# Kernel optimization log

Measured on AMD Instinct MI355X. Metric: run time of the kernel, lower is better.

The kernel has to match this reference:

```python
import jax, jax.numpy as jnp
import numpy as np

BETA = 0.25
N_E = 256
E_DIM = 1024


def setup_inputs() -> dict:
    key = jax.random.key(0)
    k1, k2, k3, k4 = jax.random.split(key, 4)
    z = jax.random.normal(k1, (16, E_DIM, 32, 32), dtype=jnp.float32)
    emb = jax.random.normal(k2, (N_E, E_DIM), dtype=jnp.float32)
    conv_w = jax.random.normal(k3, (E_DIM, E_DIM), dtype=jnp.float32) * 0.02
    conv_b = jax.random.normal(k4, (E_DIM,), dtype=jnp.float32) * 0.02
    return {"z": z, "emb": emb, "conv_w": conv_w, "conv_b": conv_b}


def reference(z, emb, conv_w, conv_b):
    # z: [B, C=e_dim, H, W] -> channels-last, flatten spatial+batch
    zp = jnp.transpose(z, (0, 2, 3, 1))          # [B, H, W, C]
    zf = zp.reshape(-1, E_DIM)                    # [N, C]
    # squared L2 distances to codebook: [N, n_e]
    d = (jnp.sum(zf * zf, axis=1, keepdims=True)
         + jnp.sum(emb * emb, axis=1)
         - 2.0 * (zf @ emb.T))
    min_idx = jnp.argmin(d, axis=1)               # [N]
    min_enc = jax.nn.one_hot(min_idx, N_E, dtype=z.dtype)  # [N, n_e]
    z_q = (min_enc @ emb).reshape(zp.shape)       # gather via matmul, as original
    # VQ commitment loss with straight-through estimator
    loss = (jnp.mean((jax.lax.stop_gradient(z_q) - zp) ** 2)
            + BETA * jnp.mean((z_q - jax.lax.stop_gradient(zp)) ** 2))
    z_q = zp + jax.lax.stop_gradient(z_q - zp)
    e_mean = jnp.mean(min_enc, axis=0)
    perplexity = jnp.exp(-jnp.sum(e_mean * jnp.log(e_mean + 1e-10)))
    # back to channels-first, then 1x1 conv (= per-pixel GEMM)
    z_q = jnp.transpose(z_q, (0, 3, 1, 2))        # [B, C, H, W]
    out = jnp.einsum('bchw,oc->bohw', z_q, conv_w) + conv_b[None, :, None, None]
    return out, loss, perplexity, min_idx
```

## Files before the change

kernel.cpp:

```cpp
#include <hip/hip_runtime.h>
#include <math.h>

#define NE 256
#define EDIM 1024
#define HW 1024
#define NPIX 16384
#define OUT_ELEMS 16777216

typedef short short8 __attribute__((ext_vector_type(8)));
typedef float f32x4 __attribute__((ext_vector_type(4)));

#define WS_HIST   0
#define WS_LOSS   1024
#define WS_ZSQ    1028
#define WS_FBITS  2048
#define WS_T      4096
#define WS_MEMSET 1052672
#define WS_CE2    1052672
#define WS_IDX    1053696
#define WS_EH     1119232
#define WS_EL     1643520
#define WS_NEED   2167808

#define DELTA 0.02f

#define WO_CE2  0
#define WO_HIST 1024
#define WO_LOSS 2048
#define WO_IDX  4096
#define WO_T    69632
#define WO_TOTAL 1118208

__device__ __forceinline__ unsigned short f2bf(float f) {
    unsigned u = __float_as_uint(f);
    unsigned r = u + 0x7FFFu + ((u >> 16) & 1u);
    return (unsigned short)(r >> 16);
}
__device__ __forceinline__ float bf2f(unsigned short h) {
    return __uint_as_float(((unsigned)h) << 16);
}

__device__ __forceinline__ void stage16(const void* g, void* l) {
    __builtin_amdgcn_global_load_lds(
        (const __attribute__((address_space(1))) unsigned int*)g,
        (__attribute__((address_space(3))) unsigned int*)l, 16, 0, 0);
}

__global__ __launch_bounds__(64) void k_prep(const float* __restrict__ emb,
                                             unsigned short* __restrict__ eh,
                                             unsigned short* __restrict__ el,
                                             float* __restrict__ ce2) {
    int j = blockIdx.x;
    int l = threadIdx.x;
    const float* row = emb + ((size_t)j << 10);
    float s = 0.f;
    #pragma unroll
    for (int i = 0; i < 4; i++) {
        float4 v = *(const float4*)(row + l * 4 + 256 * i);
        s += v.x * v.x + v.y * v.y + v.z * v.z + v.w * v.w;
        unsigned short h0 = f2bf(v.x), h1 = f2bf(v.y), h2 = f2bf(v.z), h3 = f2bf(v.w);
        uint2 hp, lp;
        hp.x = (unsigned)h0 | ((unsigned)h1 << 16);
        hp.y = (unsigned)h2 | ((unsigned)h3 << 16);
        lp.x = (unsigned)f2bf(v.x - bf2f(h0)) | ((unsigned)f2bf(v.y - bf2f(h1)) << 16);
        lp.y = (unsigned)f2bf(v.z - bf2f(h2)) | ((unsigned)f2bf(v.w - bf2f(h3)) << 16);
        *(uint2*)(eh + ((size_t)j << 10) + l * 4 + 256 * i) = hp;
        *(uint2*)(el + ((size_t)j << 10) + l * 4 + 256 * i) = lp;
    }
    #pragma unroll
    for (int m = 32; m; m >>= 1) s += __shfl_down(s, m, 64);
    if (l == 0) ce2[j] = 0.5f * s;
}

__global__ __launch_bounds__(256) void k_wT(const float* __restrict__ w,
                                            const float* __restrict__ emb,
                                            float* __restrict__ T) {
    __shared__ float wt[64 * 17];
    __shared__ float et[64 * 17];
    int t = threadIdx.x;
    int j0 = blockIdx.x * 64;
    int o0 = blockIdx.y * 64;
    int kb = blockIdx.z * 256;
    int to = t & 15, tj = t >> 4;
    float acc[4][4] = {};
    int lr = t >> 2, lk = (t & 3) * 4;
    for (int kk = kb; kk < kb + 256; kk += 16) {
        float4 wv = *(const float4*)(w + (size_t)(o0 + lr) * EDIM + kk + lk);
        float4 ev = *(const float4*)(emb + (size_t)(j0 + lr) * EDIM + kk + lk);
        __syncthreads();
        wt[lr * 17 + lk + 0] = wv.x; wt[lr * 17 + lk + 1] = wv.y;
        wt[lr * 17 + lk + 2] = wv.z; wt[lr * 17 + lk + 3] = wv.w;
        et[lr * 17 + lk + 0] = ev.x; et[lr * 17 + lk + 1] = ev.y;
        et[lr * 17 + lk + 2] = ev.z; et[lr * 17 + lk + 3] = ev.w;
        __syncthreads();
        #pragma unroll
        for (int k = 0; k < 16; k++) {
            float a[4], b[4];
            #pragma unroll
            for (int i = 0; i < 4; i++) a[i] = wt[(to * 4 + i) * 17 + k];
            #pragma unroll
            for (int i = 0; i < 4; i++) b[i] = et[(tj * 4 + i) * 17 + k];
            #pragma unroll
            for (int i = 0; i < 4; i++)
                #pragma unroll
                for (int jx = 0; jx < 4; jx++) acc[i][jx] += a[i] * b[jx];
        }
    }
    #pragma unroll
    for (int i = 0; i < 4; i++)
        #pragma unroll
        for (int jx = 0; jx < 4; jx++)
            atomicAdd(&T[(size_t)(o0 + to * 4 + i) * NE + j0 + tj * 4 + jx],
                      acc[i][jx]);
}

__global__ __launch_bounds__(256) void k_dist(
        const float* __restrict__ z, const unsigned short* __restrict__ eh,
        const unsigned short* __restrict__ el,
        const float* __restrict__ ce2,
        int* __restrict__ idx_i, float* __restrict__ idx_f,
        int* __restrict__ hist, float* __restrict__ loss_s,
        float* __restrict__ zsq_acc, unsigned int* __restrict__ fbits) {
    __shared__ unsigned short sB[4][2][256 * 32];
    int t = threadIdx.x;
    int lane = t & 63, w = t >> 6;
    int m = lane & 15, quad = lane >> 4;
    int px0 = blockIdx.x * 64;
    int b = px0 >> 10;
    const float* zp = z + (((size_t)b) << 20) + (px0 & 1023) + w * 16 + m;
    int sc = t >> 2, qp = t & 3;
    int ql = qp ^ ((sc >> 1) & 3);

    f32x4 acc[16];
    #pragma unroll
    for (int nt = 0; nt < 16; nt++) acc[nt] = (f32x4){0.f, 0.f, 0.f, 0.f};

    float zv0[8], zv1[8], zv2[8], zv3[8];
    float zsq = 0.f;
    int sq = quad ^ ((m >> 1) & 3);

#define STAGE(c, B) do {                                                        \
    int kk_ = (c) * 32;                                                         \
    _Pragma("unroll")                                                           \
    for (int i_ = 0; i_ < 4; i_++) {                                            \
        stage16(eh + (((size_t)(i_ * 64 + sc)) << 10) + kk_ + ql * 8,           \
                &sB[B][0][(i_ * 256 + w * 64) * 8]);                            \
        stage16(el + (((size_t)(i_ * 64 + sc)) << 10) + kk_ + ql * 8,           \
                &sB[B][1][(i_ * 256 + w * 64) * 8]);                            \
    } } while (0)

#define ZLOAD(c, ZV) do {                                                       \
    int kk_ = (c) * 32;                                                         \
    _Pragma("unroll")                                                           \
    for (int j_ = 0; j_ < 8; j_++)                                              \
        ZV[j_] = zp[((size_t)(kk_ + quad * 8 + j_)) << 10];                     \
    } while (0)

#define WAITV(n) do {                                                           \
    asm volatile("s_waitcnt vmcnt(" #n ")" ::: "memory");                       \
    __builtin_amdgcn_sched_barrier(0); } while (0)

#define FENCE() do {                                                            \
    asm volatile("" ::: "memory");                                              \
    __builtin_amdgcn_sched_barrier(0); } while (0)

#define BODY(c, B, ZV, PRE, B3, ZV3) do {                                       \
    __builtin_amdgcn_s_barrier();                                               \
    short8 ah, al;                                                              \
    _Pragma("unroll")                                                           \
    for (int j_ = 0; j_ < 8; j_++) {                                            \
        float zj_ = ZV[j_];                                                     \
        zsq += zj_ * zj_;                                                       \
        unsigned short h_ = f2bf(zj_);                                          \
        ((unsigned short*)&ah)[j_] = h_;                                        \
        ((unsigned short*)&al)[j_] = f2bf(zj_ - bf2f(h_));                      \
    }                                                                           \
    if (PRE) { STAGE((c) + 3, B3); ZLOAD((c) + 3, ZV3); }                       \
    _Pragma("unroll")                                                           \
    for (int nt_ = 0; nt_ < 16; nt_++) {                                        \
        short8 bh_ = *(const short8*)&sB[B][0][(nt_ * 16 + m) * 32 + sq * 8];   \
        short8 bl_ = *(const short8*)&sB[B][1][(nt_ * 16 + m) * 32 + sq * 8];   \
        acc[nt_] = __builtin_amdgcn_mfma_f32_16x16x32_bf16(ah, bh_, acc[nt_], 0, 0, 0); \
        acc[nt_] = __builtin_amdgcn_mfma_f32_16x16x32_bf16(ah, bl_, acc[nt_], 0, 0, 0); \
        acc[nt_] = __builtin_amdgcn_mfma_f32_16x16x32_bf16(al, bh_, acc[nt_], 0, 0, 0); \
    } } while (0)

    STAGE(0, 0); ZLOAD(0, zv0); FENCE();
    STAGE(1, 1); ZLOAD(1, zv1); FENCE();
    STAGE(2, 2); ZLOAD(2, zv2);

    for (int mi = 0; mi < 7; mi++) {
        WAITV(32); BODY(mi * 4 + 0, 0, zv0, 1, 3, zv3);
        WAITV(32); BODY(mi * 4 + 1, 1, zv1, 1, 0, zv0);
        WAITV(32); BODY(mi * 4 + 2, 2, zv2, 1, 1, zv1);
        WAITV(32); BODY(mi * 4 + 3, 3, zv3, 1, 2, zv2);
    }
    WAITV(32); BODY(28, 0, zv0, 1, 3, zv3);
    WAITV(32); BODY(29, 1, zv1, 0, 2, zv2);
    WAITV(16); BODY(30, 2, zv2, 0, 3, zv3);
    WAITV(0);  BODY(31, 3, zv3, 0, 0, zv0);

#undef STAGE
#undef ZLOAD
#undef WAITV
#undef FENCE
#undef BODY

    #pragma unroll
    for (int msk = 32; msk; msk >>= 1) zsq += __shfl_down(zsq, msk, 64);
    if (lane == 0) atomicAdd(zsq_acc, zsq);

    float c2v[16];
    #pragma unroll
    for (int nt = 0; nt < 16; nt++) c2v[nt] = ce2[nt * 16 + m];

    float lsum = 0.f;
    #pragma unroll
    for (int r = 0; r < 4; r++) {
        float v1 = 3.4e38f, v2 = 3.4e38f; int i1 = 0;
        #pragma unroll
        for (int nt = 0; nt < 16; nt++) {
            int code = nt * 16 + m;
            float sv = c2v[nt] - acc[nt][r];
            if (sv < v1 || (sv == v1 && code < i1)) { v2 = v1; v1 = sv; i1 = code; }
            else v2 = fminf(v2, sv);
        }
        #pragma unroll
        for (int msk = 1; msk < 16; msk <<= 1) {
            float ov1 = __shfl_xor(v1, msk, 64);
            int   oi1 = __shfl_xor(i1, msk, 64);
            float ov2 = __shfl_xor(v2, msk, 64);
            float nv2 = fminf(fminf(v2, ov2), fmaxf(v1, ov1));
            if (ov1 < v1 || (ov1 == v1 && oi1 < i1)) { v1 = ov1; i1 = oi1; }
            v2 = nv2;
        }
        if (m == 0) {
            int px = px0 + w * 16 + quad * 4 + r;
            idx_i[px] = i1;
            idx_f[px] = (float)i1;
            atomicAdd(&hist[i1], 1);
            if (v2 - v1 < DELTA)
                atomicOr(&fbits[px >> 5], 1u << (px & 31));
            lsum += v1;
        }
    }
    lsum += __shfl_xor(lsum, 16, 64);
    lsum += __shfl_xor(lsum, 32, 64);
    if (lane == 0) atomicAdd(loss_s, lsum);
}

__global__ __launch_bounds__(256) void k_cleanup(const float* __restrict__ z,
        const float* __restrict__ emb, const float* __restrict__ ce2,
        const unsigned int* __restrict__ fbits,
        int* __restrict__ idx_i, float* __restrict__ idx_f, int* __restrict__ hist) {
    __shared__ float zs[1024];
    __shared__ float rv[4];
    __shared__ int ri[4];
    int t = threadIdx.x;
    const float* er = emb + (size_t)t * EDIM;
    for (int px = blockIdx.x; px < NPIX; px += gridDim.x) {
        if (!(fbits[px >> 5] & (1u << (px & 31)))) continue;
        int b = px >> 10, p = px & 1023;
        const float* zb = z + (((size_t)b) << 20) + p;
        #pragma unroll
        for (int r = 0; r < 4; r++) {
            int c = t + 256 * r;
            zs[c] = zb[((size_t)c) << 10];
        }
        __syncthreads();
        float d0 = 0.f, d1 = 0.f, d2 = 0.f, d3 = 0.f;
        #pragma unroll 4
        for (int c = 0; c < EDIM; c += 16) {
            float4 e0 = *(const float4*)(er + c);
            float4 e1 = *(const float4*)(er + c + 4);
            float4 e2 = *(const float4*)(er + c + 8);
            float4 e3 = *(const float4*)(er + c + 12);
            d0 += e0.x * zs[c]      + e0.y * zs[c + 1]  + e0.z * zs[c + 2]  + e0.w * zs[c + 3];
            d1 += e1.x * zs[c + 4]  + e1.y * zs[c + 5]  + e1.z * zs[c + 6]  + e1.w * zs[c + 7];
            d2 += e2.x * zs[c + 8]  + e2.y * zs[c + 9]  + e2.z * zs[c + 10] + e2.w * zs[c + 11];
            d3 += e3.x * zs[c + 12] + e3.y * zs[c + 13] + e3.z * zs[c + 14] + e3.w * zs[c + 15];
        }
        float sv = ce2[t] - ((d0 + d1) + (d2 + d3));
        int bi = t;
        #pragma unroll
        for (int msk = 1; msk < 64; msk <<= 1) {
            float ov = __shfl_xor(sv, msk, 64);
            int oi = __shfl_xor(bi, msk, 64);
            if (ov < sv || (ov == sv && oi < bi)) { sv = ov; bi = oi; }
        }
        if ((t & 63) == 0) { rv[t >> 6] = sv; ri[t >> 6] = bi; }
        __syncthreads();
        if (t == 0) {
            float v = rv[0]; int ix = ri[0];
            for (int ww = 1; ww < 4; ww++)
                if (rv[ww] < v || (rv[ww] == v && ri[ww] < ix)) { v = rv[ww]; ix = ri[ww]; }
            int old = idx_i[px];
            if (ix != old) {
                idx_i[px] = ix; idx_f[px] = (float)ix;
                atomicAdd(&hist[ix], 1); atomicSub(&hist[old], 1);
            }
        }
        __syncthreads();
    }
}

__global__ __launch_bounds__(64) void k_norms(const float* __restrict__ emb,
                                              float* __restrict__ ce2) {
    int j = blockIdx.x;
    int lane = threadIdx.x;
    const float* row = emb + (size_t)j * EDIM;
    float s = 0.f;
    #pragma unroll
    for (int i = 0; i < EDIM / 64; i++) {
        float v = row[lane + 64 * i];
        s += v * v;
    }
    #pragma unroll
    for (int m = 32; m; m >>= 1) s += __shfl_down(s, m, 64);
    if (lane == 0) ce2[j] = 0.5f * s;
}

__global__ __launch_bounds__(256) void k_argmin(const float* __restrict__ z,
                                                const float* __restrict__ emb,
                                                const float* __restrict__ ce2,
                                                int* __restrict__ idx_i,
                                                float* __restrict__ idx_f,
                                                int* __restrict__ hist,
                                                float* __restrict__ loss_acc) {
    __shared__ float zt[32 * 64];
    __shared__ float et[256 * 34];
    __shared__ float znorm_s[64];
    int t = threadIdx.x;
    int n0 = blockIdx.x * 64;
    int b = n0 >> 10;
    int p0 = n0 & 1023;
    const float* zb = z + (size_t)b * EDIM * HW;
    int tc = t & 31, tp = t >> 5;
    float acc[8][8] = {};
    float znorm = 0.f;
    for (int kk = 0; kk < EDIM; kk += 32) {
        #pragma unroll
        for (int i = 0; i < 16; i++) {
            int q = t + 256 * i;
            int code = q >> 4, k2 = q & 15;
            float2 v = *(const float2*)(emb + (size_t)code * EDIM + kk + k2 * 2);
            *(float2*)(et + code * 34 + k2 * 2) = v;
        }
        #pragma unroll
        for (int i = 0; i < 4; i++) {
            int q = t + 256 * i;
            int k = q >> 5, p2 = q & 31;
            float2 v = *(const float2*)(zb + (size_t)(kk + k) * HW + p0 + p2 * 2);
            *(float2*)(zt + k * 64 + p2 * 2) = v;
        }
        __syncthreads();
        if (t < 64) {
            #pragma unroll
            for (int k = 0; k < 32; k++) { float zz = zt[k * 64 + t]; znorm += zz * zz; }
        }
        #pragma unroll 4
        for (int k2 = 0; k2 < 16; k2++) {
            float2 ev[8], za[4], zb2[4];
            #pragma unroll
            for (int u = 0; u < 8; u++)
                ev[u] = *(float2*)(et + (tc + 32 * u) * 34 + k2 * 2);
            #pragma unroll
            for (int j = 0; j < 4; j++)
                za[j] = *(float2*)(zt + (2 * k2) * 64 + tp * 8 + 2 * j);
            #pragma unroll
            for (int j = 0; j < 4; j++)
                zb2[j] = *(float2*)(zt + (2 * k2 + 1) * 64 + tp * 8 + 2 * j);
            #pragma unroll
            for (int p = 0; p < 8; p++) {
                float z0 = (p & 1) ? za[p >> 1].y : za[p >> 1].x;
                float z1 = (p & 1) ? zb2[p >> 1].y : zb2[p >> 1].x;
                #pragma unroll
                for (int u = 0; u < 8; u++)
                    acc[p][u] += z0 * ev[u].x + z1 * ev[u].y;
            }
        }
        __syncthreads();
    }
    if (t < 64) znorm_s[t] = znorm;
    float minv[8];
    int mini[8];
    #pragma unroll
    for (int p = 0; p < 8; p++) { minv[p] = 3.4e38f; mini[p] = 0; }
    #pragma unroll
    for (int u = 0; u < 8; u++) {
        int code = tc + 32 * u;
        float cc2 = ce2[code];
        #pragma unroll
        for (int p = 0; p < 8; p++) {
            float s = cc2 - acc[p][u];
            if (s < minv[p] || (s == minv[p] && code < mini[p])) { minv[p] = s; mini[p] = code; }
        }
    }
    #pragma unroll
    for (int m = 1; m < 32; m <<= 1) {
        #pragma unroll
        for (int p = 0; p < 8; p++) {
            float ov = __shfl_xor(minv[p], m, 64);
            int oi = __shfl_xor(mini[p], m, 64);
            if (ov < minv[p] || (ov == minv[p] && oi < mini[p])) { minv[p] = ov; mini[p] = oi; }
        }
    }
    __syncthreads();
    if (tc == 0) {
        float dsum = 0.f;
        #pragma unroll
        for (int p = 0; p < 8; p++) {
            int lp = tp * 8 + p;
            int n = n0 + lp;
            idx_i[n] = mini[p];
            idx_f[n] = (float)mini[p];
            dsum += znorm_s[lp] + 2.f * minv[p];
            atomicAdd(&hist[mini[p]], 1);
        }
        atomicAdd(loss_acc, dsum);
    }
}

__global__ __launch_bounds__(256) void k_scatter(const float* __restrict__ T,
                                                 const float* __restrict__ bias,
                                                 const int* __restrict__ idx,
                                                 float* __restrict__ out) {
    __shared__ float Ts[16 * 256];
    __shared__ float bs[16];
    int t = threadIdx.x;
    int o0 = blockIdx.x * 16;
    int b = blockIdx.y;
    #pragma unroll
    for (int r = 0; r < 16; r++)
        Ts[r * 256 + t] = T[(size_t)(o0 + r) * NE + t];
    if (t < 16) bs[t] = bias[o0 + t];
    __syncthreads();
    int4 i4 = *(const int4*)(idx + b * HW + t * 4);
    #pragma unroll
    for (int r = 0; r < 16; r++) {
        const float* Tr = Ts + r * 256;
        float bb = bs[r];
        float4 v;
        v.x = Tr[i4.x] + bb;
        v.y = Tr[i4.y] + bb;
        v.z = Tr[i4.z] + bb;
        v.w = Tr[i4.w] + bb;
        *(float4*)(out + ((size_t)(b * EDIM + o0 + r) * HW) + t * 4) = v;
    }
}

__global__ __launch_bounds__(256) void k_final_new(const int* __restrict__ hist,
                                                   const float* __restrict__ loss_s,
                                                   const float* __restrict__ zsq,
                                                   float* __restrict__ out) {
    __shared__ float red[4];
    int t = threadIdx.x;
    float em = (float)hist[t] * (1.0f / 16384.0f);
    float v = em * logf(em + 1e-10f);
    #pragma unroll
    for (int m = 32; m; m >>= 1) v += __shfl_down(v, m, 64);
    if ((t & 63) == 0) red[t >> 6] = v;
    __syncthreads();
    if (t == 0) {
        float s = red[0] + red[1] + red[2] + red[3];
        out[OUT_ELEMS] = (zsq[0] + 2.f * loss_s[0]) * 1.25f / 16777216.f;
        out[OUT_ELEMS + 1] = expf(-s);
    }
}

__global__ __launch_bounds__(256) void k_final_old(const int* __restrict__ hist,
                                                   const float* __restrict__ loss_acc,
                                                   float* __restrict__ out) {
    __shared__ float red[4];
    int t = threadIdx.x;
    float em = (float)hist[t] * (1.0f / 16384.0f);
    float v = em * logf(em + 1e-10f);
    #pragma unroll
    for (int m = 32; m; m >>= 1) v += __shfl_down(v, m, 64);
    if ((t & 63) == 0) red[t >> 6] = v;
    __syncthreads();
    if (t == 0) {
        float s = red[0] + red[1] + red[2] + red[3];
        out[OUT_ELEMS] = loss_acc[0] * 1.25f / 16777216.f;
        out[OUT_ELEMS + 1] = expf(-s);
    }
}

extern "C" void kernel_launch(void* const* d_in, const int* in_sizes, int n_in,
                              void* d_out, int out_size, void* d_ws, size_t ws_size,
                              hipStream_t stream) {
    (void)in_sizes; (void)n_in; (void)out_size;
    const float* z      = (const float*)d_in[0];
    const float* emb    = (const float*)d_in[1];
    const float* conv_w = (const float*)d_in[2];
    const float* conv_b = (const float*)d_in[3];
    float* out = (float*)d_out;

    if (ws_size >= WS_NEED) {
        int*   hist     = (int*)((char*)d_ws + WS_HIST);
        float* loss_s   = (float*)((char*)d_ws + WS_LOSS);
        float* zsq      = (float*)((char*)d_ws + WS_ZSQ);
        unsigned int* fbits = (unsigned int*)((char*)d_ws + WS_FBITS);
        float* T        = (float*)((char*)d_ws + WS_T);
        float* ce2      = (float*)((char*)d_ws + WS_CE2);
        int*   idx_i    = (int*)((char*)d_ws + WS_IDX);
        unsigned short* eh = (unsigned short*)((char*)d_ws + WS_EH);
        unsigned short* el = (unsigned short*)((char*)d_ws + WS_EL);
        float* idx_f = out + OUT_ELEMS + 2;

        hipMemsetAsync(d_ws, 0, WS_MEMSET, stream);
        k_prep<<<NE, 64, 0, stream>>>(emb, eh, el, ce2);
        k_wT<<<dim3(4, 16, 4), 256, 0, stream>>>(conv_w, emb, T);
        k_dist<<<256, 256, 0, stream>>>(z, eh, el, ce2, idx_i, idx_f,
                                        hist, loss_s, zsq, fbits);
        k_cleanup<<<256, 256, 0, stream>>>(z, emb, ce2, fbits, idx_i, idx_f, hist);
        k_scatter<<<dim3(64, 16), 256, 0, stream>>>(T, conv_b, idx_i, out);
        k_final_new<<<1, 256, 0, stream>>>(hist, loss_s, zsq, out);
    } else {
        float* ce2      = (float*)((char*)d_ws + WO_CE2);
        int*   hist     = (int*)((char*)d_ws + WO_HIST);
        float* loss_acc = (float*)((char*)d_ws + WO_LOSS);
        int*   idx_i    = (int*)((char*)d_ws + WO_IDX);
        float* T        = (float*)((char*)d_ws + WO_T);
        float* idx_f = out + OUT_ELEMS + 2;

        hipMemsetAsync(d_ws, 0, WO_TOTAL, stream);
        k_norms<<<NE, 64, 0, stream>>>(emb, ce2);
        k_wT<<<dim3(4, 16, 4), 256, 0, stream>>>(conv_w, emb, T);
        k_argmin<<<256, 256, 0, stream>>>(z, emb, ce2, idx_i, idx_f, hist, loss_acc);
        k_scatter<<<dim3(64, 16), 256, 0, stream>>>(T, conv_b, idx_i, out);
        k_final_old<<<1, 256, 0, stream>>>(hist, loss_acc, out);
    }
}
```

Measured before the change: 253.1 us.

## Switch distance GEMM to 32x32x16 MFMA with split-codebook waves and triple buffering

The distance kernel now uses 32x32x16 bf16 MFMAs instead of 16x16x32. Each pair of waves splits the 256 codes into two halves of 128 over the same 32 pixels, and the two partial top-2 argmins are merged through shared memory. The LDS pipeline drops from four stages to three with a two-ahead prefetch, which frees shared memory and registers. The goal is fewer LDS fragment reads per FLOP and higher MFMA throughput, at the cost of an extra __syncthreads, a cross-half merge step and a shallower prefetch depth.

Result: slower. 260.8 us (+3.1%).

```diff
diff --git a/kernel.cpp b/kernel.cpp
--- a/kernel.cpp
+++ b/kernel.cpp
@@ -9,6 +9,7 @@
 
 typedef short short8 __attribute__((ext_vector_type(8)));
 typedef float f32x4 __attribute__((ext_vector_type(4)));
+typedef float f32x16 __attribute__((ext_vector_type(16)));
 
 #define WS_HIST   0
 #define WS_LOSS   1024
@@ -121,40 +122,48 @@
         int* __restrict__ idx_i, float* __restrict__ idx_f,
         int* __restrict__ hist, float* __restrict__ loss_s,
         float* __restrict__ zsq_acc, unsigned int* __restrict__ fbits) {
-    __shared__ unsigned short sB[4][2][256 * 32];
+    __shared__ unsigned short sB3[3][2][256 * 32];
+    __shared__ float v1h[2][64], v2h[2][64];
+    __shared__ int   i1h[2][64];
     int t = threadIdx.x;
     int lane = t & 63, w = t >> 6;
-    int m = lane & 15, quad = lane >> 4;
+    int cid = lane & 31, lh = lane >> 5;
+    int half = w & 1;
+    int pxt = w >> 1;
+    int c_base = half << 7;
+    int cswz = (cid >> 1) & 3;
     int px0 = blockIdx.x * 64;
     int b = px0 >> 10;
-    const float* zp = z + (((size_t)b) << 20) + (px0 & 1023) + w * 16 + m;
+    const float* zp = z + (((size_t)b) << 20) + (px0 & 1023) + pxt * 32 + cid;
     int sc = t >> 2, qp = t & 3;
     int ql = qp ^ ((sc >> 1) & 3);
 
-    f32x4 acc[16];
-    #pragma unroll
-    for (int nt = 0; nt < 16; nt++) acc[nt] = (f32x4){0.f, 0.f, 0.f, 0.f};
-
-    float zv0[8], zv1[8], zv2[8], zv3[8];
+    f32x16 acc[4];
+    #pragma unroll
+    for (int nt = 0; nt < 4; nt++)
+        #pragma unroll
+        for (int i = 0; i < 16; i++) acc[nt][i] = 0.f;
+
+    float zvA[16], zvB[16], zvC[16];
     float zsq = 0.f;
-    int sq = quad ^ ((m >> 1) & 3);
 
 #define STAGE(c, B) do {                                                        \
     int kk_ = (c) * 32;                                                         \
     _Pragma("unroll")                                                           \
     for (int i_ = 0; i_ < 4; i_++) {                                            \
         stage16(eh + (((size_t)(i_ * 64 + sc)) << 10) + kk_ + ql * 8,           \
-                &sB[B][0][(i_ * 256 + w * 64) * 8]);                            \
+                &sB3[B][0][(i_ * 256 + w * 64) * 8]);                           \
         stage16(el + (((size_t)(i_ * 64 + sc)) << 10) + kk_ + ql * 8,           \
-                &sB[B][1][(i_ * 256 + w * 64) * 8]);                            \
+                &sB3[B][1][(i_ * 256 + w * 64) * 8]);                           \
     } } while (0)
 
 #define ZLOAD(c, ZV) do {                                                       \
     int kk_ = (c) * 32;                                                         \
     _Pragma("unroll")                                                           \
-    for (int j_ = 0; j_ < 8; j_++)                                              \
-        ZV[j_] = zp[((size_t)(kk_ + quad * 8 + j_)) << 10];                     \
-    } while (0)
+    for (int j_ = 0; j_ < 8; j_++) {                                            \
+        ZV[j_]     = zp[((size_t)(kk_ + lh * 8 + j_)) << 10];                   \
+        ZV[8 + j_] = zp[((size_t)(kk_ + 16 + lh * 8 + j_)) << 10];              \
+    } } while (0)
 
 #define WAITV(n) do {                                                           \
     asm volatile("s_waitcnt vmcnt(" #n ")" ::: "memory");                       \
@@ -164,41 +173,48 @@
     asm volatile("" ::: "memory");                                              \
     __builtin_amdgcn_sched_barrier(0); } while (0)
 
-#define BODY(c, B, ZV, PRE, B3, ZV3) do {                                       \
+#define BODY(c, B, ZV, PRE, B2, ZV2) do {                                       \
     __builtin_amdgcn_s_barrier();                                               \
-    short8 ah, al;                                                              \
+    FENCE();                                                                    \
+    short8 ah0, al0, ah1, al1;                                                  \
     _Pragma("unroll")                                                           \
     for (int j_ = 0; j_ < 8; j_++) {                                            \
-        float zj_ = ZV[j_];                                                     \
-        zsq += zj_ * zj_;                                                       \
-        unsigned short h_ = f2bf(zj_);                                          \
-        ((unsigned short*)&ah)[j_] = h_;                                        \
-        ((unsigned short*)&al)[j_] = f2bf(zj_ - bf2f(h_));                      \
+        float z0_ = ZV[j_], z1_ = ZV[8 + j_];                                   \
+        zsq += z0_ * z0_ + z1_ * z1_;                                           \
+        unsigned short h0_ = f2bf(z0_), h1_ = f2bf(z1_);                        \
+        ((unsigned short*)&ah0)[j_] = h0_;                                      \
+        ((unsigned short*)&al0)[j_] = f2bf(z0_ - bf2f(h0_));                    \
+        ((unsigned short*)&ah1)[j_] = h1_;                                      \
+        ((unsigned short*)&al1)[j_] = f2bf(z1_ - bf2f(h1_));                    \
     }                                                                           \
-    if (PRE) { STAGE((c) + 3, B3); ZLOAD((c) + 3, ZV3); }                       \
+    if (PRE) { STAGE((c) + 2, B2); ZLOAD((c) + 2, ZV2); }                       \
     _Pragma("unroll")                                                           \
-    for (int nt_ = 0; nt_ < 16; nt_++) {                                        \
-        short8 bh_ = *(const short8*)&sB[B][0][(nt_ * 16 + m) * 32 + sq * 8];   \
-        short8 bl_ = *(const short8*)&sB[B][1][(nt_ * 16 + m) * 32 + sq * 8];   \
-        acc[nt_] = __builtin_amdgcn_mfma_f32_16x16x32_bf16(ah, bh_, acc[nt_], 0, 0, 0); \
-        acc[nt_] = __builtin_amdgcn_mfma_f32_16x16x32_bf16(ah, bl_, acc[nt_], 0, 0, 0); \
-        acc[nt_] = __builtin_amdgcn_mfma_f32_16x16x32_bf16(al, bh_, acc[nt_], 0, 0, 0); \
+    for (int t_ = 0; t_ < 4; t_++) {                                            \
+        int crow_ = (c_base + t_ * 32 + cid) * 32;                              \
+        int sp0_ = lh ^ cswz;                                                   \
+        int sp1_ = (2 + lh) ^ cswz;                                             \
+        short8 bh0_ = *(const short8*)&sB3[B][0][crow_ + sp0_ * 8];             \
+        short8 bl0_ = *(const short8*)&sB3[B][1][crow_ + sp0_ * 8];             \
+        short8 bh1_ = *(const short8*)&sB3[B][0][crow_ + sp1_ * 8];             \
+        short8 bl1_ = *(const short8*)&sB3[B][1][crow_ + sp1_ * 8];             \
+        acc[t_] = __builtin_amdgcn_mfma_f32_32x32x16_bf16(ah0, bh0_, acc[t_], 0, 0, 0); \
+        acc[t_] = __builtin_amdgcn_mfma_f32_32x32x16_bf16(ah0, bl0_, acc[t_], 0, 0, 0); \
+        acc[t_] = __builtin_amdgcn_mfma_f32_32x32x16_bf16(al0, bh0_, acc[t_], 0, 0, 0); \
+        acc[t_] = __builtin_amdgcn_mfma_f32_32x32x16_bf16(ah1, bh1_, acc[t_], 0, 0, 0); \
+        acc[t_] = __builtin_amdgcn_mfma_f32_32x32x16_bf16(ah1, bl1_, acc[t_], 0, 0, 0); \
+        acc[t_] = __builtin_amdgcn_mfma_f32_32x32x16_bf16(al1, bh1_, acc[t_], 0, 0, 0); \
     } } while (0)
 
-    STAGE(0, 0); ZLOAD(0, zv0); FENCE();
-    STAGE(1, 1); ZLOAD(1, zv1); FENCE();
-    STAGE(2, 2); ZLOAD(2, zv2);
-
-    for (int mi = 0; mi < 7; mi++) {
-        WAITV(32); BODY(mi * 4 + 0, 0, zv0, 1, 3, zv3);
-        WAITV(32); BODY(mi * 4 + 1, 1, zv1, 1, 0, zv0);
-        WAITV(32); BODY(mi * 4 + 2, 2, zv2, 1, 1, zv1);
-        WAITV(32); BODY(mi * 4 + 3, 3, zv3, 1, 2, zv2);
-    }
-    WAITV(32); BODY(28, 0, zv0, 1, 3, zv3);
-    WAITV(32); BODY(29, 1, zv1, 0, 2, zv2);
-    WAITV(16); BODY(30, 2, zv2, 0, 3, zv3);
-    WAITV(0);  BODY(31, 3, zv3, 0, 0, zv0);
+    STAGE(0, 0); ZLOAD(0, zvA); FENCE();
+    STAGE(1, 1); ZLOAD(1, zvB);
+
+    for (int mi = 0; mi < 10; mi++) {
+        WAITV(24); BODY(mi * 3 + 0, 0, zvA, 1, 2, zvC);
+        WAITV(24); BODY(mi * 3 + 1, 1, zvB, 1, 0, zvA);
+        WAITV(24); BODY(mi * 3 + 2, 2, zvC, 1, 1, zvB);
+    }
+    WAITV(24); BODY(30, 0, zvA, 0, 1, zvB);
+    WAITV(0);  BODY(31, 1, zvB, 0, 2, zvC);
 
 #undef STAGE
 #undef ZLOAD
@@ -208,25 +224,24 @@
 
     #pragma unroll
     for (int msk = 32; msk; msk >>= 1) zsq += __shfl_down(zsq, msk, 64);
-    if (lane == 0) atomicAdd(zsq_acc, zsq);
-
-    float c2v[16];
-    #pragma unroll
-    for (int nt = 0; nt < 16; nt++) c2v[nt] = ce2[nt * 16 + m];
-
-    float lsum = 0.f;
-    #pragma unroll
-    for (int r = 0; r < 4; r++) {
+    if (half == 0 && lane == 0) atomicAdd(zsq_acc, zsq);
+
+    float c2v[4];
+    #pragma unroll
+    for (int t_ = 0; t_ < 4; t_++) c2v[t_] = ce2[c_base + t_ * 32 + cid];
+
+    #pragma unroll
+    for (int r = 0; r < 16; r++) {
         float v1 = 3.4e38f, v2 = 3.4e38f; int i1 = 0;
         #pragma unroll
-        for (int nt = 0; nt < 16; nt++) {
-            int code = nt * 16 + m;
-            float sv = c2v[nt] - acc[nt][r];
+        for (int t_ = 0; t_ < 4; t_++) {
+            int code = c_base + t_ * 32 + cid;
+            float sv = c2v[t_] - acc[t_][r];
             if (sv < v1 || (sv == v1 && code < i1)) { v2 = v1; v1 = sv; i1 = code; }
             else v2 = fminf(v2, sv);
         }
         #pragma unroll
-        for (int msk = 1; msk < 16; msk <<= 1) {
+        for (int msk = 1; msk < 32; msk <<= 1) {
             float ov1 = __shfl_xor(v1, msk, 64);
             int   oi1 = __shfl_xor(i1, msk, 64);
             float ov2 = __shfl_xor(v2, msk, 64);
@@ -234,19 +249,38 @@
             if (ov1 < v1 || (ov1 == v1 && oi1 < i1)) { v1 = ov1; i1 = oi1; }
             v2 = nv2;
         }
-        if (m == 0) {
-            int px = px0 + w * 16 + quad * 4 + r;
-            idx_i[px] = i1;
-            idx_f[px] = (float)i1;
-            atomicAdd(&hist[i1], 1);
-            if (v2 - v1 < DELTA)
-                atomicOr(&fbits[px >> 5], 1u << (px & 31));
-            lsum += v1;
-        }
-    }
-    lsum += __shfl_xor(lsum, 16, 64);
-    lsum += __shfl_xor(lsum, 32, 64);
-    if (lane == 0) atomicAdd(loss_s, lsum);
+        if (cid == 0) {
+            int pl = pxt * 32 + (r & 3) + 8 * (r >> 2) + 4 * lh;
+            v1h[half][pl] = v1; v2h[half][pl] = v2; i1h[half][pl] = i1;
+        }
+    }
+    __syncthreads();
+    if (half == 1) {
+        float lsum = 0.f;
+        if (cid == 0) {
+            #pragma unroll
+            for (int r = 0; r < 16; r++) {
+                int pl = pxt * 32 + (r & 3) + 8 * (r >> 2) + 4 * lh;
+                float va = v1h[0][pl], v2a = v2h[0][pl];
+                int   ia = i1h[0][pl];
+                float vb = v1h[1][pl], v2b = v2h[1][pl];
+                int   ib = i1h[1][pl];
+                float v2m = fminf(fminf(v2a, v2b), fmaxf(va, vb));
+                float v1; int i1;
+                if (vb < va) { v1 = vb; i1 = ib; }
+                else         { v1 = va; i1 = ia; }
+                int px = px0 + pl;
+                idx_i[px] = i1;
+                idx_f[px] = (float)i1;
+                atomicAdd(&hist[i1], 1);
+                if (v2m - v1 < DELTA)
+                    atomicOr(&fbits[px >> 5], 1u << (px & 31));
+                lsum += v1;
+            }
+        }
+        lsum += __shfl_xor(lsum, 32, 64);
+        if (lane == 0) atomicAdd(loss_s, lsum);
+    }
 }
 
 __global__ __launch_bounds__(256) void k_cleanup(const float* __restrict__ z,
```
